# Optimization experiments

Measured on AMD Instinct MI355X. Metric: run time of the kernel, lower is better.

The kernel has to match this reference:

```python
import jax, jax.numpy as jnp
import numpy as np

DIM = 1024
N_HEADS = 16
HEAD_DIM = DIM // N_HEADS
MAX_SEQ = 2048
BATCH = 4
SEQ = 2048


def _rope_tables(seq_len, head_dim):
    inv_freq = 1.0 / (10000.0 ** (jnp.arange(0, head_dim, 2, dtype=jnp.float32) / head_dim))
    t = jnp.arange(seq_len, dtype=jnp.float32)
    freqs = jnp.outer(t, inv_freq)            # [S, D/2]
    emb = jnp.concatenate([freqs, freqs], axis=-1)  # [S, D]
    return jnp.cos(emb), jnp.sin(emb)


def setup_inputs() -> dict:
    key = jax.random.key(0)
    kx, kq, kk, kv, ko = jax.random.split(key, 5)
    s = 1.0 / np.sqrt(DIM)
    x = jax.random.normal(kx, (BATCH, SEQ, DIM), dtype=jnp.float32)
    Wq = jax.random.normal(kq, (DIM, DIM), dtype=jnp.float32) * s
    Wk = jax.random.normal(kk, (DIM, DIM), dtype=jnp.float32) * s
    Wv = jax.random.normal(kv, (DIM, DIM), dtype=jnp.float32) * s
    Wo = jax.random.normal(ko, (DIM, DIM), dtype=jnp.float32) * s
    cos, sin = _rope_tables(SEQ, HEAD_DIM)
    mask = jnp.tril(jnp.ones((SEQ, SEQ), dtype=bool))[None, None]  # [1,1,S,S] causal
    return {"x": x, "Wq": Wq, "Wk": Wk, "Wv": Wv, "Wo": Wo,
            "cos": cos, "sin": sin, "mask": mask}


def _rotate_half(t):
    t1, t2 = jnp.split(t, 2, axis=-1)
    return jnp.concatenate([-t2, t1], axis=-1)


def reference(x, Wq, Wk, Wv, Wo, cos, sin, mask):
    B, S, _ = x.shape
    # projections (torch Linear: y = x @ W.T)
    q = (x @ Wq.T).reshape(B, S, N_HEADS, HEAD_DIM)
    k = (x @ Wk.T).reshape(B, S, N_HEADS, HEAD_DIM)
    v = (x @ Wv.T).reshape(B, S, N_HEADS, HEAD_DIM)
    # RoPE on [B,S,H,D]: cos/sin broadcast over batch and heads
    c = cos[None, :S, None, :]
    s_ = sin[None, :S, None, :]
    q = q * c + _rotate_half(q) * s_
    k = k * c + _rotate_half(k) * s_
    # attention, heads-major
    scale = HEAD_DIM ** -0.5
    attn = jnp.einsum('bqhd,bkhd->bhqk', q, k) * scale
    attn = jnp.where(mask, attn, -jnp.inf)
    attn = jax.nn.softmax(attn, axis=-1)
    out = jnp.einsum('bhqk,bkhd->bqhd', attn, v).reshape(B, S, DIM)
    return out @ Wo.T
```

## Files before the change

kernel.cpp:

```cpp
#include <hip/hip_runtime.h>
#include <hip/hip_bf16.h>
#include <stdint.h>

typedef __bf16 bf16;
typedef __bf16 bf16x4 __attribute__((ext_vector_type(4)));
typedef __bf16 bf16x8 __attribute__((ext_vector_type(8)));
typedef float f32x4 __attribute__((ext_vector_type(4)));

static constexpr int DIMM  = 1024;
static constexpr int NHEADS = 16;
static constexpr int HDIM  = 64;
static constexpr int SEQL  = 2048;
static constexpr int NB    = 4;
static constexpr int MTOT  = NB * SEQL;
static constexpr float LOG2E = 1.4426950408889634f;

__device__ __forceinline__ int swz(int row, int kc) {
    return row * 128 + ((kc ^ (row & 7)) << 4);
}

__device__ __forceinline__ void gl_lds16(const void* g, void* l) {
    __builtin_amdgcn_global_load_lds(
        (const __attribute__((address_space(1))) unsigned int*)g,
        (__attribute__((address_space(3))) unsigned int*)l,
        16, 0, 0);
}

__device__ __forceinline__ bf16x8 cvt8(f32x4 a, f32x4 b) {
    bf16x8 r;
    r[0] = (bf16)a[0]; r[1] = (bf16)a[1]; r[2] = (bf16)a[2]; r[3] = (bf16)a[3];
    r[4] = (bf16)b[0]; r[5] = (bf16)b[1]; r[6] = (bf16)b[2]; r[7] = (bf16)b[3];
    return r;
}

__global__ __launch_bounds__(256)
void cvt_kernel(const float* __restrict__ x,  const float* __restrict__ Wq,
                const float* __restrict__ Wk, const float* __restrict__ Wv,
                const float* __restrict__ Wo,
                bf16* __restrict__ xb,  bf16* __restrict__ Wqb,
                bf16* __restrict__ Wkb, bf16* __restrict__ Wvb,
                bf16* __restrict__ Wob)
{
    const size_t NX = (size_t)MTOT * DIMM;
    const size_t NW = (size_t)DIMM * DIMM;
    size_t i = ((size_t)blockIdx.x * 256 + threadIdx.x) * 8;
    const float* src; bf16* dst; size_t off;
    if (i < NX) { src = x; dst = xb; off = i; }
    else {
        size_t j = i - NX;
        int wsel = (int)(j >> 20);
        off = j & (NW - 1);
        if      (wsel == 0) { src = Wq; dst = Wqb; }
        else if (wsel == 1) { src = Wk; dst = Wkb; }
        else if (wsel == 2) { src = Wv; dst = Wvb; }
        else                { src = Wo; dst = Wob; }
    }
    f32x4 a = *(const f32x4*)(src + off);
    f32x4 b = *(const f32x4*)(src + off + 4);
    *(bf16x8*)(dst + off) = cvt8(a, b);
}

__global__ __launch_bounds__(256, 2)
void qkv_kernel(const bf16* __restrict__ xb,
                const bf16* __restrict__ Wqb, const bf16* __restrict__ Wkb,
                const bf16* __restrict__ Wvb,
                const float* __restrict__ cosT, const float* __restrict__ sinT,
                bf16* __restrict__ qb, bf16* __restrict__ kb, bf16* __restrict__ vTb)
{
    __shared__ __align__(16) bf16 As[2][128 * 32];
    __shared__ __align__(16) bf16 Bq[2][128 * 32];
    __shared__ __align__(16) bf16 Bk[2][128 * 32];
    __shared__ __align__(16) bf16 Bv[2][128 * 32];

    const int bid = (int)blockIdx.x;
    const int bn  = (bid & 7) * 128;
    const int bm  = (bid >> 3) * 128;

    const int tid  = threadIdx.x;
    const int lane = tid & 63;
    const int w    = tid >> 6;
    const int l15  = lane & 15;
    const int lg   = lane >> 4;
    const int wm   = (w >> 1) * 64;
    const int wn   = (w & 1) * 64;

    f32x4 acc[3][4][4];
    #pragma unroll
    for (int w3 = 0; w3 < 3; ++w3)
        #pragma unroll
        for (int mf = 0; mf < 4; ++mf)
            #pragma unroll
            for (int nf = 0; nf < 4; ++nf)
                acc[w3][mf][nf] = f32x4{0.f, 0.f, 0.f, 0.f};

    const int c0  = w * 2;
    const int rp0 = lane >> 3;
    const int tt  = (lane & 7) ^ rp0;
    const int rgo = (tt >> 2) << 6;
    const int kq  = (tt & 3) * 8;

    auto stage = [&](int t, int buf) {
        const int k0 = t * 32;
        #pragma unroll
        for (int i = 0; i < 2; ++i) {
            const int c  = c0 + i;
            const int rg = c * 8 + rp0 + rgo;
            const size_t am = (size_t)(bm + rg) * DIMM + k0 + kq;
            const size_t an = (size_t)(bn + rg) * DIMM + k0 + kq;
            gl_lds16(xb  + am, &As[buf][c * 512]);
            gl_lds16(Wqb + an, &Bq[buf][c * 512]);
            gl_lds16(Wkb + an, &Bk[buf][c * 512]);
            gl_lds16(Wvb + an, &Bv[buf][c * 512]);
        }
    };

    auto rd = [&](const bf16* base, int row) {
        return *(const bf16x8*)((const char*)base +
            (row & 63) * 128 + (((((row >> 6) << 2) | lg) ^ (row & 7)) << 4));
    };

    auto compute = [&](int buf) {
        bf16x8 af[4];
        #pragma unroll
        for (int mf = 0; mf < 4; ++mf)
            af[mf] = rd(As[buf], wm + mf * 16 + l15);
        const bf16* bsel[3] = {Bq[buf], Bk[buf], Bv[buf]};
        __builtin_amdgcn_s_setprio(1);
        #pragma unroll
        for (int w3 = 0; w3 < 3; ++w3) {
            bf16x8 bfr[4];
            #pragma unroll
            for (int nf = 0; nf < 4; ++nf)
                bfr[nf] = rd(bsel[w3], wn + nf * 16 + l15);
            #pragma unroll
            for (int mf = 0; mf < 4; ++mf)
                #pragma unroll
                for (int nf = 0; nf < 4; ++nf)
                    acc[w3][mf][nf] = __builtin_amdgcn_mfma_f32_16x16x32_bf16(
                        af[mf], bfr[nf], acc[w3][mf][nf], 0, 0, 0);
        }
        __builtin_amdgcn_s_setprio(0);
    };

    stage(0, 0);
    #pragma unroll 1
    for (int t = 0; t < 31; ++t) {
        stage(t + 1, (t + 1) & 1);
        asm volatile("s_waitcnt vmcnt(8)" ::: "memory");
        __builtin_amdgcn_s_barrier();
        __builtin_amdgcn_sched_barrier(0);
        compute(t & 1);
        __builtin_amdgcn_sched_barrier(0);
        __builtin_amdgcn_s_barrier();
    }
    asm volatile("s_waitcnt vmcnt(0)" ::: "memory");
    __builtin_amdgcn_s_barrier();
    __builtin_amdgcn_sched_barrier(0);
    compute(1);

    #pragma unroll
    for (int mf = 0; mf < 4; ++mf) {
        #pragma unroll
        for (int nf = 0; nf < 4; ++nf) {
            int n = bn + wn + nf * 16 + l15;
            int h = n >> 6;
            int d = n & 63;
            float sign = (d < 32) ? -1.f : 1.f;
            #pragma unroll
            for (int r = 0; r < 4; ++r) {
                int m = bm + wm + mf * 16 + lg * 4 + r;
                int b = m >> 11, s = m & 2047;
                float c  = cosT[s * 64 + d];
                float sv = sinT[s * 64 + d];
                size_t o_qk = ((size_t)((b * NHEADS + h) * SEQL + s)) * HDIM + d;
                float q0 = acc[0][mf][nf][r], q1 = acc[0][mf][nf ^ 2][r];
                float k0v = acc[1][mf][nf][r], k1 = acc[1][mf][nf ^ 2][r];
                qb[o_qk] = (bf16)((q0 * c + sign * q1 * sv) * (0.125f * LOG2E));
                kb[o_qk] = (bf16)(k0v * c + sign * k1 * sv);
                vTb[((size_t)((b * NHEADS + h) * HDIM + d)) * SEQL + s] = (bf16)acc[2][mf][nf][r];
            }
        }
    }
}

__global__ __launch_bounds__(256, 3)
void attn_kernel(bf16* __restrict__ qb, const bf16* __restrict__ kb,
                 const bf16* __restrict__ vTb)
{
    __shared__ __align__(16) bf16 Ks[2][64 * 64];
    __shared__ __align__(16) bf16 Vs[2][64 * 64];
    __shared__ __align__(16) bf16 Pl[4][32 * 64];

    const int bh  = blockIdx.x;
    const int qt  = 15 - (int)blockIdx.y;
    const int tid = threadIdx.x;
    const int lane = tid & 63, w = tid >> 6;
    const int l15 = lane & 15, lg = lane >> 4;

    bf16*       Qp = qb  + (size_t)bh * SEQL * HDIM;
    const bf16* Kp = kb  + (size_t)bh * SEQL * HDIM;
    const bf16* Vp = vTb + (size_t)bh * HDIM * SEQL;

    const int q0  = qt * 128 + w * 32;
    const int njt = 2 * qt + 2;

    bf16x8 qf[2][2];
    #pragma unroll
    for (int mf = 0; mf < 2; ++mf)
        #pragma unroll
        for (int ks = 0; ks < 2; ++ks)
            qf[mf][ks] = *(const bf16x8*)(Qp + (size_t)(q0 + mf * 16 + l15) * HDIM + ks * 32 + lg * 8);

    bf16x8 ones;
    #pragma unroll
    for (int e = 0; e < 8; ++e) ones[e] = (bf16)1.0f;

    f32x4 oacc[4][2];
    f32x4 lacc[2];
    #pragma unroll
    for (int mf = 0; mf < 2; ++mf) lacc[mf] = f32x4{0.f, 0.f, 0.f, 0.f};
    #pragma unroll
    for (int nd = 0; nd < 4; ++nd)
        #pragma unroll
        for (int mf = 0; mf < 2; ++mf)
            oacc[nd][mf] = f32x4{0.f, 0.f, 0.f, 0.f};

    char* Pw = (char*)Pl[w];
    const int l7 = l15 & 7;
    const int srow0 = tid >> 3;
    const int skc   = tid & 7;

    bf16x8 kr[2], vr[2];
    auto issue = [&](int j) {
        const int kk0 = j * 64;
        #pragma unroll
        for (int c = 0; c < 2; ++c) {
            int row = c * 32 + srow0;
            kr[c] = *(const bf16x8*)(Kp + (size_t)(kk0 + row) * HDIM + skc * 8);
            vr[c] = *(const bf16x8*)(Vp + (size_t)row * SEQL + kk0 + skc * 8);
        }
    };
    auto commit = [&](int b) {
        #pragma unroll
        for (int c = 0; c < 2; ++c) {
            int row = c * 32 + srow0;
            *(bf16x8*)((char*)Ks[b] + swz(row, skc)) = kr[c];
            *(bf16x8*)((char*)Vs[b] + swz(row, skc)) = vr[c];
        }
    };

    issue(0);
    commit(0);
    __syncthreads();

    for (int j = 0; j < njt; ++j) {
        const int kk0 = j * 64;
        const int buf = j & 1;
        const bool more = (j + 1 < njt);
        if (more) issue(j + 1);

        f32x4 sacc[4][2];
        #pragma unroll
        for (int nf = 0; nf < 4; ++nf)
            #pragma unroll
            for (int mf = 0; mf < 2; ++mf)
                sacc[nf][mf] = f32x4{0.f, 0.f, 0.f, 0.f};
        #pragma unroll
        for (int ks = 0; ks < 2; ++ks) {
            bf16x8 kf[4];
            #pragma unroll
            for (int nf = 0; nf < 4; ++nf)
                kf[nf] = *(const bf16x8*)((const char*)Ks[buf] + swz(nf * 16 + l15, ks * 4 + lg));
            #pragma unroll
            for (int nf = 0; nf < 4; ++nf)
                #pragma unroll
                for (int mf = 0; mf < 2; ++mf)
                    sacc[nf][mf] = __builtin_amdgcn_mfma_f32_16x16x32_bf16(
                        kf[nf], qf[mf][ks], sacc[nf][mf], 0, 0, 0);
        }

        const bool nm = (kk0 + 63 > q0);
        #pragma unroll
        for (int nf = 0; nf < 4; ++nf) {
            #pragma unroll
            for (int mf = 0; mf < 2; ++mf) {
                bf16x4 pb;
                #pragma unroll
                for (int r = 0; r < 4; ++r) {
                    float s = sacc[nf][mf][r];
                    if (nm) {
                        int kv = kk0 + nf * 16 + lg * 4 + r;
                        int qq = q0 + mf * 16 + l15;
                        if (kv > qq) s = -1.0e30f;
                    }
                    pb[r] = (bf16)exp2f(s);
                }
                *(bf16x4*)(Pw + (mf * 16 + l15) * 128
                              + (((2 * nf + (lg >> 1)) ^ l7) << 4) + (lg & 1) * 8) = pb;
            }
        }

        #pragma unroll
        for (int ks = 0; ks < 2; ++ks) {
            bf16x8 pf[2], vf[4];
            #pragma unroll
            for (int mf = 0; mf < 2; ++mf)
                pf[mf] = *(const bf16x8*)(Pw + (mf * 16 + l15) * 128
                                             + (((ks * 4 + lg) ^ l7) << 4));
            #pragma unroll
            for (int nd = 0; nd < 4; ++nd)
                vf[nd] = *(const bf16x8*)((const char*)Vs[buf] + swz(nd * 16 + l15, ks * 4 + lg));
            #pragma unroll
            for (int mf = 0; mf < 2; ++mf)
                lacc[mf] = __builtin_amdgcn_mfma_f32_16x16x32_bf16(
                    ones, pf[mf], lacc[mf], 0, 0, 0);
            #pragma unroll
            for (int nd = 0; nd < 4; ++nd)
                #pragma unroll
                for (int mf = 0; mf < 2; ++mf)
                    oacc[nd][mf] = __builtin_amdgcn_mfma_f32_16x16x32_bf16(
                        vf[nd], pf[mf], oacc[nd][mf], 0, 0, 0);
        }

        if (more) {
            commit(buf ^ 1);
            __syncthreads();
        }
    }

    float inv[2] = {1.f / lacc[0][0], 1.f / lacc[1][0]};
    #pragma unroll
    for (int nd = 0; nd < 4; ++nd)
        #pragma unroll
        for (int mf = 0; mf < 2; ++mf) {
            bf16x4 o4;
            #pragma unroll
            for (int r = 0; r < 4; ++r)
                o4[r] = (bf16)(oacc[nd][mf][r] * inv[mf]);
            int s = q0 + mf * 16 + l15;
            int d = nd * 16 + lg * 4;
            *(bf16x4*)(Qp + (size_t)s * HDIM + d) = o4;
        }
}

__global__ __launch_bounds__(256, 2)
void oproj_kernel(const bf16* __restrict__ O, const bf16* __restrict__ Wob,
                  float* __restrict__ outp)
{
    __shared__ __align__(16) bf16 Bs[2][128 * 32];

    const int bm = (int)blockIdx.x * 128;
    const int bn = (int)blockIdx.y * 128;

    const int tid  = threadIdx.x;
    const int lane = tid & 63;
    const int w    = tid >> 6;
    const int l15  = lane & 15;
    const int lg   = lane >> 4;
    const int wm   = (w >> 1) * 64;
    const int wn   = (w & 1) * 64;

    f32x4 acc[4][4];
    #pragma unroll
    for (int mf = 0; mf < 4; ++mf)
        #pragma unroll
        for (int nf = 0; nf < 4; ++nf)
            acc[mf][nf] = f32x4{0.f, 0.f, 0.f, 0.f};

    const int c0  = w * 2;
    const int rp0 = lane >> 3;
    const int tt  = (lane & 7) ^ rp0;
    const int rgo = (tt >> 2) << 6;
    const int kq  = (tt & 3) * 8;

    auto stageB = [&](int t, int buf) {
        const int k0 = t * 32;
        #pragma unroll
        for (int i = 0; i < 2; ++i) {
            const int c  = c0 + i;
            const int rg = c * 8 + rp0 + rgo;
            gl_lds16(Wob + (size_t)(bn + rg) * DIMM + k0 + kq, &Bs[buf][c * 512]);
        }
    };

    auto loadA = [&](bf16x8 (&dst)[4], int t) {
        const int k0 = t * 32;
        #pragma unroll
        for (int mf = 0; mf < 4; ++mf) {
            int m = bm + wm + mf * 16 + l15;
            int b = m >> 11, s = m & 2047;
            int k = k0 + lg * 8;
            int h = k >> 6, dd = k & 63;
            dst[mf] = *(const bf16x8*)(O + ((size_t)((b * NHEADS + h) * SEQL + s)) * HDIM + dd);
        }
    };

    auto rd = [&](const bf16* base, int row) {
        return *(const bf16x8*)((const char*)base +
            (row & 63) * 128 + (((((row >> 6) << 2) | lg) ^ (row & 7)) << 4));
    };

    auto compute = [&](int buf, const bf16x8 (&af)[4]) {
        bf16x8 bfr[4];
        #pragma unroll
        for (int nf = 0; nf < 4; ++nf)
            bfr[nf] = rd(Bs[buf], wn + nf * 16 + l15);
        #pragma unroll
        for (int mf = 0; mf < 4; ++mf)
            #pragma unroll
            for (int nf = 0; nf < 4; ++nf)
                acc[mf][nf] = __builtin_amdgcn_mfma_f32_16x16x32_bf16(
                    af[mf], bfr[nf], acc[mf][nf], 0, 0, 0);
    };

    bf16x8 aA[4], aB[4];

    stageB(0, 0);
    __builtin_amdgcn_sched_barrier(0);
    loadA(aA, 0);
    __builtin_amdgcn_sched_barrier(0);

    auto step = [&](bf16x8 (&cur)[4], bf16x8 (&nxt)[4], int t) {
        stageB(t + 1, (t + 1) & 1);
        __builtin_amdgcn_sched_barrier(0);
        asm volatile("s_waitcnt vmcnt(6)" ::: "memory");
        __builtin_amdgcn_s_barrier();
        __builtin_amdgcn_sched_barrier(0);
        loadA(nxt, t + 1);
        compute(t & 1, cur);
        __builtin_amdgcn_sched_barrier(0);
        __builtin_amdgcn_s_barrier();
    };

    #pragma unroll 1
    for (int tp = 0; tp < 15; ++tp) {
        step(aA, aB, 2 * tp);
        step(aB, aA, 2 * tp + 1);
    }
    step(aA, aB, 30);
    asm volatile("s_waitcnt vmcnt(0)" ::: "memory");
    __builtin_amdgcn_s_barrier();
    __builtin_amdgcn_sched_barrier(0);
    compute(1, aB);

    #pragma unroll
    for (int mf = 0; mf < 4; ++mf)
        #pragma unroll
        for (int nf = 0; nf < 4; ++nf) {
            int n = bn + wn + nf * 16 + l15;
            #pragma unroll
            for (int r = 0; r < 4; ++r) {
                int m = bm + wm + mf * 16 + lg * 4 + r;
                outp[(size_t)m * DIMM + n] = acc[mf][nf][r];
            }
        }
}

extern "C" void kernel_launch(void* const* d_in, const int* in_sizes, int n_in,
                              void* d_out, int out_size, void* d_ws, size_t ws_size,
                              hipStream_t stream)
{
    const float* x    = (const float*)d_in[0];
    const float* Wq   = (const float*)d_in[1];
    const float* Wk   = (const float*)d_in[2];
    const float* Wv   = (const float*)d_in[3];
    const float* Wo   = (const float*)d_in[4];
    const float* cosT = (const float*)d_in[5];
    const float* sinT = (const float*)d_in[6];

    const size_t NELEM = (size_t)MTOT * DIMM;
    const size_t NW    = (size_t)DIMM * DIMM;
    bf16* qb  = (bf16*)d_ws;
    bf16* kb  = qb + NELEM;
    bf16* vT  = kb + NELEM;
    bf16* xb  = vT + NELEM;
    bf16* Wqb = xb + NELEM;
    bf16* Wkb = Wqb + NW;
    bf16* Wvb = Wkb + NW;
    bf16* Wob = Wvb + NW;

    dim3 blk(256);
    cvt_kernel<<<dim3(6144), blk, 0, stream>>>(x, Wq, Wk, Wv, Wo,
                                               xb, Wqb, Wkb, Wvb, Wob);

    qkv_kernel<<<dim3(512), blk, 0, stream>>>(xb, Wqb, Wkb, Wvb, cosT, sinT,
                                              qb, kb, vT);

    dim3 g2(NB * NHEADS, SEQL / 128);
    attn_kernel<<<g2, blk, 0, stream>>>(qb, kb, vT);

    dim3 g3(MTOT / 128, DIMM / 128);
    oproj_kernel<<<g3, blk, 0, stream>>>(qb, Wob, (float*)d_out);
}
```

Before: 174.7 us.

## Feed P to PV MFMA directly from registers using 16x16x16 bf16 MFMA

Removes the per-wave LDS staging buffer for the softmax probabilities. The S accumulator layout is reused directly as the B operand of the older 16x16x16 bf16 MFMA, and V fragments are read from LDS to match that layout. This drops the LDS write, the readback and the shared memory they used, which allows occupancy to rise to 4 blocks. In exchange it issues twice as many smaller MFMAs with half-K throughput and makes more, narrower LDS reads of V.

Result: slower. 233.6 us (+33.7%).

```diff
diff --git a/kernel.cpp b/kernel.cpp
--- a/kernel.cpp
+++ b/kernel.cpp
@@ -6,6 +6,7 @@
 typedef __bf16 bf16x4 __attribute__((ext_vector_type(4)));
 typedef __bf16 bf16x8 __attribute__((ext_vector_type(8)));
 typedef float f32x4 __attribute__((ext_vector_type(4)));
+typedef short s16x4 __attribute__((ext_vector_type(4)));
 
 static constexpr int DIMM  = 1024;
 static constexpr int NHEADS = 16;
@@ -31,6 +32,10 @@
     r[0] = (bf16)a[0]; r[1] = (bf16)a[1]; r[2] = (bf16)a[2]; r[3] = (bf16)a[3];
     r[4] = (bf16)b[0]; r[5] = (bf16)b[1]; r[6] = (bf16)b[2]; r[7] = (bf16)b[3];
     return r;
+}
+
+__device__ __forceinline__ f32x4 mfma16(s16x4 a, s16x4 b, f32x4 c) {
+    return __builtin_amdgcn_mfma_f32_16x16x16bf16_1k(a, b, c, 0, 0, 0);
 }
 
 __global__ __launch_bounds__(256)
@@ -183,19 +188,19 @@
     }
 }
 
-__global__ __launch_bounds__(256, 3)
+__global__ __launch_bounds__(256, 4)
 void attn_kernel(bf16* __restrict__ qb, const bf16* __restrict__ kb,
                  const bf16* __restrict__ vTb)
 {
     __shared__ __align__(16) bf16 Ks[2][64 * 64];
     __shared__ __align__(16) bf16 Vs[2][64 * 64];
-    __shared__ __align__(16) bf16 Pl[4][32 * 64];
 
     const int bh  = blockIdx.x;
     const int qt  = 15 - (int)blockIdx.y;
     const int tid = threadIdx.x;
     const int lane = tid & 63, w = tid >> 6;
     const int l15 = lane & 15, lg = lane >> 4;
+    const int l7  = l15 & 7;
 
     bf16*       Qp = qb  + (size_t)bh * SEQL * HDIM;
     const bf16* Kp = kb  + (size_t)bh * SEQL * HDIM;
@@ -211,9 +216,9 @@
         for (int ks = 0; ks < 2; ++ks)
             qf[mf][ks] = *(const bf16x8*)(Qp + (size_t)(q0 + mf * 16 + l15) * HDIM + ks * 32 + lg * 8);
 
-    bf16x8 ones;
-    #pragma unroll
-    for (int e = 0; e < 8; ++e) ones[e] = (bf16)1.0f;
+    s16x4 onesA;
+    #pragma unroll
+    for (int e = 0; e < 4; ++e) onesA[e] = (short)0x3F80;
 
     f32x4 oacc[4][2];
     f32x4 lacc[2];
@@ -225,8 +230,6 @@
         for (int mf = 0; mf < 2; ++mf)
             oacc[nd][mf] = f32x4{0.f, 0.f, 0.f, 0.f};
 
-    char* Pw = (char*)Pl[w];
-    const int l7 = l15 & 7;
     const int srow0 = tid >> 3;
     const int skc   = tid & 7;
 
@@ -280,11 +283,11 @@
         }
 
         const bool nm = (kk0 + 63 > q0);
+        s16x4 pB[4][2];
         #pragma unroll
         for (int nf = 0; nf < 4; ++nf) {
             #pragma unroll
             for (int mf = 0; mf < 2; ++mf) {
-                bf16x4 pb;
                 #pragma unroll
                 for (int r = 0; r < 4; ++r) {
                     float s = sacc[nf][mf][r];
@@ -293,33 +296,27 @@
                         int qq = q0 + mf * 16 + l15;
                         if (kv > qq) s = -1.0e30f;
                     }
-                    pb[r] = (bf16)exp2f(s);
+                    bf16 pbv = (bf16)exp2f(s);
+                    pB[nf][mf][r] = __builtin_bit_cast(short, pbv);
                 }
-                *(bf16x4*)(Pw + (mf * 16 + l15) * 128
-                              + (((2 * nf + (lg >> 1)) ^ l7) << 4) + (lg & 1) * 8) = pb;
             }
         }
 
         #pragma unroll
-        for (int ks = 0; ks < 2; ++ks) {
-            bf16x8 pf[2], vf[4];
+        for (int nf = 0; nf < 4; ++nf) {
+            s16x4 vfr[4];
+            #pragma unroll
+            for (int nd = 0; nd < 4; ++nd)
+                vfr[nd] = *(const s16x4*)((const char*)Vs[buf] + (nd * 16 + l15) * 128
+                              + (((2 * nf + (lg >> 1)) ^ l7) << 4) + (lg & 1) * 8);
             #pragma unroll
             for (int mf = 0; mf < 2; ++mf)
-                pf[mf] = *(const bf16x8*)(Pw + (mf * 16 + l15) * 128
-                                             + (((ks * 4 + lg) ^ l7) << 4));
-            #pragma unroll
-            for (int nd = 0; nd < 4; ++nd)
-                vf[nd] = *(const bf16x8*)((const char*)Vs[buf] + swz(nd * 16 + l15, ks * 4 + lg));
-            #pragma unroll
-            for (int mf = 0; mf < 2; ++mf)
-                lacc[mf] = __builtin_amdgcn_mfma_f32_16x16x32_bf16(
-                    ones, pf[mf], lacc[mf], 0, 0, 0);
+                lacc[mf] = mfma16(onesA, pB[nf][mf], lacc[mf]);
             #pragma unroll
             for (int nd = 0; nd < 4; ++nd)
                 #pragma unroll
                 for (int mf = 0; mf < 2; ++mf)
-                    oacc[nd][mf] = __builtin_amdgcn_mfma_f32_16x16x32_bf16(
-                        vf[nd], pf[mf], oacc[nd][mf], 0, 0, 0);
+                    oacc[nd][mf] = mfma16(vfr[nd], pB[nf][mf], oacc[nd][mf]);
         }
 
         if (more) {
```
